# Optimization experiments

Measured on AMD Instinct MI355X. Metric: run time of the kernel, lower is better.

Reference implementation:

```python
import jax, jax.numpy as jnp
import numpy as np
from jax import lax

EPS = 1e-12
ALPHA = 20.0
TEMP = 10.0
TAU = 0.45
LAMBDA_N = 0.3
REP_W = 0.15
MOMENTUM = 0.9
N_SINK_ITER = 3


def _norm(x):
    # F.normalize(p=2, dim=1, eps=1e-12)
    return x / jnp.maximum(jnp.linalg.norm(x, axis=-1, keepdims=True), EPS)


def sinkhorn(sim, alpha=ALPHA, n_iterations=N_SINK_ITER):
    Q = jnp.exp(alpha * sim).T  # [K, B]
    K, B = Q.shape
    Q = Q / jnp.sum(Q)
    for _ in range(n_iterations):
        Q = Q / (jnp.sum(Q, axis=1, keepdims=True) * K)
        Q = Q / (jnp.sum(Q, axis=0, keepdims=True) * B)
    return (Q * B).T  # [B, K]


def update_negative_centers(n_feats, positive_center, negative_centers):
    # all under no_grad in the original
    nf = _norm(n_feats)
    pos = _norm(positive_center)
    sim_to_pos = (nf @ pos.T)[:, 0]                       # [Nn]
    keep = sim_to_pos < 0.7
    negc = _norm(negative_centers)
    sim = nf @ negc.T                                     # [Nn, K]
    assign = jnp.argmax(sim, axis=1)
    K = negative_centers.shape[0]
    onehot = jax.nn.one_hot(assign, K, dtype=n_feats.dtype) * keep[:, None].astype(n_feats.dtype)
    counts = jnp.sum(onehot, axis=0)                      # [K]
    sums = onehot.T @ n_feats                             # [K, D] masked per-cluster sums of raw feats
    means = sums / jnp.maximum(counts[:, None], 1.0)
    new_center = _norm(means)
    lerped = negative_centers + (new_center - negative_centers) * (1.0 - MOMENTUM)
    lerped = lerped / jnp.maximum(jnp.linalg.norm(lerped, axis=1, keepdims=True), EPS)
    # update only clusters with >=3 assigned kept features (skips everything if keep.sum()==0)
    return jnp.where((counts >= 3.0)[:, None], lerped, negative_centers)


def setup_inputs() -> dict:
    key = jax.random.key(0)
    ks = jax.random.split(key, 6)
    dim, n_proxies, n_centers = 512, 1024, 4
    return {
        'p_feats': jax.random.normal(ks[0], (16384, dim), jnp.float32),
        'u_feats': jax.random.normal(ks[1], (65536, dim), jnp.float32),
        'n_feats': jax.random.normal(ks[2], (32768, dim), jnp.float32),
        'positive_center': _norm(jax.random.normal(ks[3], (1, dim), jnp.float32)),
        'proxy_u': jax.random.normal(ks[4], (n_proxies, dim), jnp.float32),
        'negative_centers': _norm(jax.random.normal(ks[5], (n_centers, dim), jnp.float32)),
    }


def reference(p_feats, u_feats, n_feats, positive_center, proxy_u, negative_centers):
    pos = lax.stop_gradient(positive_center)   # requires_grad=False param
    negc0 = lax.stop_gradient(negative_centers)  # buffer

    # l_loss: mean(1 - cos(pos, p_feats))
    dist = _norm(pos) @ _norm(p_feats).T       # [1, Np]
    l_loss = jnp.mean(1.0 - dist)

    # EMA update of negative centers (no_grad)
    negc = lax.stop_gradient(update_negative_centers(lax.stop_gradient(n_feats), pos, negc0))

    # n branch: self-distillation on negative centers
    sim_n = _norm(n_feats) @ _norm(negc).T     # [Nn, K]
    target_n = jax.nn.softmax(sim_n, axis=1)
    loss_n = -jnp.mean(jnp.sum(target_n * jax.nn.log_softmax(sim_n, axis=1), axis=1))

    # pseudo-label branch on u_feats vs negative centers (sinkhorn targets, detached)
    sim_u_neg = _norm(u_feats) @ _norm(negc).T  # [Nu, K]
    soft_assign = sinkhorn(lax.stop_gradient(sim_u_neg))
    loss_pseudo = -jnp.mean(jnp.sum(soft_assign * jax.nn.log_softmax(sim_u_neg, axis=1), axis=1))

    n_loss = (loss_n + loss_pseudo) / 2.0

    # u branch vs learnable proxies
    u_similarity = _norm(u_feats) @ _norm(proxy_u).T  # [Nu, P]
    u_target = sinkhorn(lax.stop_gradient(u_similarity))
    u_loss = -jnp.mean(jnp.sum(u_target * jax.nn.log_softmax(u_similarity * TEMP, axis=1), axis=1))

    # repulsion
    sim_np = (_norm(negc) @ _norm(pos).T)[:, 0]       # [K]
    rep_np = -jnp.mean(jnp.log(jnp.clip(1.0 - sim_np, 1e-6, None)))
    nc = _norm(negc)
    sim_nn = nc @ nc.T                                 # [K, K]
    K = negc.shape[0]
    offdiag = ~jnp.eye(K, dtype=bool)
    logs = jnp.where(offdiag, jnp.log(jnp.clip(1.0 - sim_nn, 1e-6, None)), 0.0)
    rep_nn = -jnp.sum(logs) / (K * K - K)
    repulsion_loss = rep_np + 0.1 * rep_nn

    cls_loss = TAU * l_loss + LAMBDA_N * n_loss + (0.55 - TAU) * u_loss + REP_W * repulsion_loss
    return cls_loss, l_loss, u_loss, n_loss, repulsion_loss
```

## Files before the change

### kernel.cpp

```cpp
#include <hip/hip_runtime.h>
#include <hip/hip_bf16.h>

typedef __attribute__((ext_vector_type(8))) short short8;
typedef __attribute__((ext_vector_type(8))) unsigned short ushort8;
typedef __attribute__((ext_vector_type(4))) float f32x4;

#define EPSN 1e-12f
#define GN 1024
#define GK 512

__device__ __forceinline__ float bf2f(unsigned short h) {
  union { unsigned int u; float f; } c; c.u = ((unsigned int)h) << 16; return c.f;
}
__device__ __forceinline__ unsigned short f2bf(float f) {
  union { float f; unsigned int u; } c; c.f = f;
  unsigned int u = c.u;
  return (unsigned short)((u + 0x7fffu + ((u >> 16) & 1u)) >> 16);
}
__device__ __forceinline__ float wredsum(float v) {
  v += __shfl_xor(v, 32); v += __shfl_xor(v, 16); v += __shfl_xor(v, 8);
  v += __shfl_xor(v, 4);  v += __shfl_xor(v, 2);  v += __shfl_xor(v, 1);
  return v;
}

#define GLL(g, l) __builtin_amdgcn_global_load_lds( \
    (const __attribute__((address_space(1))) unsigned int*)(g), \
    (__attribute__((address_space(3))) unsigned int*)(l), 16, 0, 0)

__global__ void k_prep(const float* __restrict__ pc, const float* __restrict__ nc,
                       float* __restrict__ pos_hat, float* __restrict__ negc0_hat) {
  int tid = threadIdx.x, lane = tid & 63, w = tid >> 6;
  const float* src = (w == 0) ? pc : (nc + (w - 1) * 512);
  float* dst = (w == 0) ? pos_hat : (negc0_hat + (w - 1) * 512);
  float4 a = *(const float4*)(src + lane * 8);
  float4 b = *(const float4*)(src + lane * 8 + 4);
  float x[8] = {a.x,a.y,a.z,a.w,b.x,b.y,b.z,b.w};
  float ss = 0.f;
  #pragma unroll
  for (int j = 0; j < 8; j++) ss += x[j]*x[j];
  ss = wredsum(ss);
  float inv = 1.f / fmaxf(sqrtf(ss), EPSN);
  #pragma unroll
  for (int j = 0; j < 8; j++) dst[lane*8+j] = x[j]*inv;
}

__global__ __launch_bounds__(256) void k_redcol(const float* __restrict__ P, float* __restrict__ R,
                                                int nrows, int ncols) {
  __shared__ float lred[64];
  int tid = threadIdx.x, lane = tid & 63, w = tid >> 6;
  int colg = blockIdx.x * 16;
  int ci = tid & 15;
  int r0 = tid >> 4;
  float s = 0.f;
  for (int r = r0; r < nrows; r += 16)
    s += P[(size_t)r * ncols + colg + ci];
  s += __shfl_xor(s, 16); s += __shfl_xor(s, 32);
  if (lane < 16) lred[w * 16 + lane] = s;
  __syncthreads();
  if (tid < 16) R[colg + tid] = lred[tid] + lred[16 + tid] + lred[32 + tid] + lred[48 + tid];
}

__global__ __launch_bounds__(256) void k_rownormP(const float* __restrict__ X,
                                                  unsigned short* __restrict__ Y,
                                                  float* __restrict__ invn, int rows) {
  int lane = threadIdx.x & 63;
  int w0 = blockIdx.x * 4 + (threadIdx.x >> 6);
  int nw = gridDim.x * 4;
  for (int row = w0; row < rows; row += nw) {
    const float* src = X + (size_t)row * 512 + lane * 8;
    float4 a = *(const float4*)src;
    float4 b = *(const float4*)(src + 4);
    float x[8] = {a.x,a.y,a.z,a.w,b.x,b.y,b.z,b.w};
    float ss = 0.f;
    #pragma unroll
    for (int j = 0; j < 8; j++) ss += x[j]*x[j];
    ss = wredsum(ss);
    float inv = 1.f / fmaxf(sqrtf(ss), EPSN);
    if (lane == 0) invn[row] = inv;
    ushort8 o;
    #pragma unroll
    for (int j = 0; j < 8; j++) o[j] = f2bf(x[j]);
    *(ushort8*)(Y + (size_t)row * 512 + lane * 8) = o;
  }
}

__global__ __launch_bounds__(256) void k_ploss(const float* __restrict__ PF, const float* __restrict__ ph_g,
                                               float* __restrict__ PlossP) {
  __shared__ float lred[4];
  int tid = threadIdx.x, lane = tid & 63, w = tid >> 6;
  float ph[8];
  #pragma unroll
  for (int j = 0; j < 8; j++) ph[j] = ph_g[lane*8+j];
  float lsum = 0.f;
  int row0 = blockIdx.x * 32;
  for (int rr = w; rr < 32; rr += 4) {
    int row = row0 + rr;
    const float* src = PF + (size_t)row * 512 + lane * 8;
    float4 a = *(const float4*)src;
    float4 b = *(const float4*)(src + 4);
    float x[8] = {a.x,a.y,a.z,a.w,b.x,b.y,b.z,b.w};
    float ss = 0.f, dp = 0.f;
    #pragma unroll
    for (int j = 0; j < 8; j++) { ss += x[j]*x[j]; dp += x[j]*ph[j]; }
    ss = wredsum(ss); dp = wredsum(dp);
    if (lane == 0) lsum += dp / fmaxf(sqrtf(ss), EPSN);
  }
  if (lane == 0) lred[w] = lsum;
  __syncthreads();
  if (tid == 0) PlossP[blockIdx.x] = lred[0]+lred[1]+lred[2]+lred[3];
}

__global__ __launch_bounds__(256) void k_nstats(const float* __restrict__ NF, const float* __restrict__ ph_g,
                                                const float* __restrict__ nch0, float* __restrict__ inv_n,
                                                float* __restrict__ CntP, float* __restrict__ SumP) {
  __shared__ float fl[8192];
  __shared__ float cb[16];
  int tid = threadIdx.x, lane = tid & 63, w = tid >> 6;
  float ph[8], nh[4][8];
  #pragma unroll
  for (int j = 0; j < 8; j++) ph[j] = ph_g[lane*8+j];
  #pragma unroll
  for (int c = 0; c < 4; c++)
    #pragma unroll
    for (int j = 0; j < 8; j++) nh[c][j] = nch0[c*512 + lane*8 + j];
  float acc[4][8];
  float cnt[4] = {0.f,0.f,0.f,0.f};
  #pragma unroll
  for (int c = 0; c < 4; c++)
    #pragma unroll
    for (int j = 0; j < 8; j++) acc[c][j] = 0.f;
  int row0 = blockIdx.x * 64;
  for (int rr = w; rr < 64; rr += 4) {
    int row = row0 + rr;
    const float* src = NF + (size_t)row * 512 + lane * 8;
    float4 a = *(const float4*)src;
    float4 b = *(const float4*)(src + 4);
    float x[8] = {a.x,a.y,a.z,a.w,b.x,b.y,b.z,b.w};
    float ss = 0.f, dp = 0.f, dn[4] = {0.f,0.f,0.f,0.f};
    #pragma unroll
    for (int j = 0; j < 8; j++) {
      ss += x[j]*x[j]; dp += x[j]*ph[j];
      #pragma unroll
      for (int c = 0; c < 4; c++) dn[c] += x[j]*nh[c][j];
    }
    ss = wredsum(ss); dp = wredsum(dp);
    #pragma unroll
    for (int c = 0; c < 4; c++) dn[c] = wredsum(dn[c]);
    float inv = 1.f / fmaxf(sqrtf(ss), EPSN);
    if (lane == 0) inv_n[row] = inv;
    float sp = dp * inv;
    float s0 = dn[0]*inv, s1 = dn[1]*inv, s2 = dn[2]*inv, s3 = dn[3]*inv;
    int am = 0; float best = s0;
    if (s1 > best) { best = s1; am = 1; }
    if (s2 > best) { best = s2; am = 2; }
    if (s3 > best) { best = s3; am = 3; }
    float kf = (sp < 0.7f) ? 1.f : 0.f;
    #pragma unroll
    for (int c = 0; c < 4; c++) {
      float m = (am == c) ? kf : 0.f;
      #pragma unroll
      for (int j = 0; j < 8; j++) acc[c][j] += m * x[j];
      if (lane == 0) cnt[c] += m;
    }
  }
  #pragma unroll
  for (int c = 0; c < 4; c++)
    #pragma unroll
    for (int j = 0; j < 8; j++) fl[w*2048 + c*512 + lane*8 + j] = acc[c][j];
  if (lane == 0) {
    #pragma unroll
    for (int c = 0; c < 4; c++) cb[w*4+c] = cnt[c];
  }
  __syncthreads();
  for (int q = tid; q < 2048; q += 256)
    SumP[(size_t)blockIdx.x * 2048 + q] = fl[q] + fl[2048+q] + fl[4096+q] + fl[6144+q];
  if (tid < 4) CntP[blockIdx.x * 4 + tid] = cb[tid] + cb[4+tid] + cb[8+tid] + cb[12+tid];
}

__global__ void k_center(const float* __restrict__ CntP, const float* __restrict__ sums,
                         const float* __restrict__ negc_raw, const float* __restrict__ pos_hat,
                         float* __restrict__ negc_hat, float* __restrict__ scal) {
  __shared__ float hbuf[2048];
  __shared__ float spn[4];
  __shared__ float snn[16];
  int tid = threadIdx.x, lane = tid & 63, c = tid >> 6;
  float cs = 0.f;
  for (int r = lane; r < 512; r += 64) cs += CntP[r*4 + c];
  float cnt = wredsum(cs);
  float x[8], raw[8], ph[8];
  #pragma unroll
  for (int j = 0; j < 8; j++) {
    x[j] = sums[c*512 + lane*8 + j] / fmaxf(cnt, 1.f);
    raw[j] = negc_raw[c*512 + lane*8 + j];
    ph[j] = pos_hat[lane*8 + j];
  }
  float ss = 0.f;
  #pragma unroll
  for (int j = 0; j < 8; j++) ss += x[j]*x[j];
  ss = wredsum(ss);
  float n1 = fmaxf(sqrtf(ss), EPSN);
  #pragma unroll
  for (int j = 0; j < 8; j++) x[j] = raw[j] + (x[j]/n1 - raw[j]) * 0.1f;
  ss = 0.f;
  #pragma unroll
  for (int j = 0; j < 8; j++) ss += x[j]*x[j];
  ss = wredsum(ss);
  float n2 = fmaxf(sqrtf(ss), EPSN);
  bool upd = (cnt >= 3.0f);
  #pragma unroll
  for (int j = 0; j < 8; j++) x[j] = upd ? (x[j]/n2) : raw[j];
  ss = 0.f;
  #pragma unroll
  for (int j = 0; j < 8; j++) ss += x[j]*x[j];
  ss = wredsum(ss);
  float n3 = fmaxf(sqrtf(ss), EPSN);
  float dp = 0.f;
  #pragma unroll
  for (int j = 0; j < 8; j++) {
    x[j] = x[j] / n3;
    negc_hat[c*512 + lane*8 + j] = x[j];
    hbuf[c*512 + lane*8 + j] = x[j];
    dp += x[j] * ph[j];
  }
  dp = wredsum(dp);
  if (lane == 0) spn[c] = dp;
  __syncthreads();
  float d4[4] = {0.f,0.f,0.f,0.f};
  #pragma unroll
  for (int c2 = 0; c2 < 4; c2++) {
    float d = 0.f;
    #pragma unroll
    for (int j = 0; j < 8; j++) d += x[j] * hbuf[c2*512 + lane*8 + j];
    d4[c2] = wredsum(d);
  }
  if (lane == 0) {
    #pragma unroll
    for (int c2 = 0; c2 < 4; c2++) snn[c*4 + c2] = d4[c2];
  }
  __syncthreads();
  if (tid == 0) {
    float rep_np = 0.f;
    for (int i = 0; i < 4; i++) rep_np += logf(fmaxf(1.f - spn[i], 1e-6f));
    rep_np = -rep_np * 0.25f;
    float rep_nn = 0.f;
    for (int i = 0; i < 4; i++)
      for (int j2 = 0; j2 < 4; j2++)
        if (i != j2) rep_nn += logf(fmaxf(1.f - snn[i*4+j2], 1e-6f));
    rep_nn = -rep_nn / 12.f;
    scal[4] = rep_np + 0.1f * rep_nn;
  }
}

__global__ __launch_bounds__(256) void k_nloss(const float* __restrict__ NF, const float* __restrict__ inv_n,
                                               const float* __restrict__ nch, float* __restrict__ NlossP) {
  __shared__ float lred[4];
  int tid = threadIdx.x, lane = tid & 63, w = tid >> 6;
  float nh[4][8];
  #pragma unroll
  for (int c = 0; c < 4; c++)
    #pragma unroll
    for (int j = 0; j < 8; j++) nh[c][j] = nch[c*512 + lane*8 + j];
  float lsum = 0.f;
  int row0 = blockIdx.x * 32;
  for (int rr = w; rr < 32; rr += 4) {
    int row = row0 + rr;
    const float* src = NF + (size_t)row * 512 + lane * 8;
    float4 a = *(const float4*)src;
    float4 b = *(const float4*)(src + 4);
    float x[8] = {a.x,a.y,a.z,a.w,b.x,b.y,b.z,b.w};
    float dn[4] = {0.f,0.f,0.f,0.f};
    #pragma unroll
    for (int j = 0; j < 8; j++)
      #pragma unroll
      for (int c = 0; c < 4; c++) dn[c] += x[j]*nh[c][j];
    #pragma unroll
    for (int c = 0; c < 4; c++) dn[c] = wredsum(dn[c]);
    if (lane == 0) {
      float inv = inv_n[row];
      float s0 = dn[0]*inv, s1 = dn[1]*inv, s2 = dn[2]*inv, s3 = dn[3]*inv;
      float mx = fmaxf(fmaxf(s0,s1), fmaxf(s2,s3));
      float e0 = __expf(s0-mx), e1 = __expf(s1-mx), e2 = __expf(s2-mx), e3 = __expf(s3-mx);
      float Z = e0+e1+e2+e3;
      lsum += (mx + logf(Z)) - (e0*s0+e1*s1+e2*s2+e3*s3)/Z;
    }
  }
  if (lane == 0) lred[w] = lsum;
  __syncthreads();
  if (tid == 0) NlossP[blockIdx.x] = lred[0]+lred[1]+lred[2]+lred[3];
}

__global__ __launch_bounds__(256) void k_upass(const float* __restrict__ U, const float* __restrict__ nch,
                                               float* __restrict__ SU, float* __restrict__ UPp,
                                               unsigned short* __restrict__ Uh, float* __restrict__ invU) {
  __shared__ float ub[16];
  int tid = threadIdx.x, lane = tid & 63, w = tid >> 6;
  float nh[4][8];
  #pragma unroll
  for (int c = 0; c < 4; c++)
    #pragma unroll
    for (int j = 0; j < 8; j++) nh[c][j] = nch[c*512 + lane*8 + j];
  float eacc[4] = {0.f,0.f,0.f,0.f};
  int row0 = blockIdx.x * 32;
  for (int rr = w; rr < 32; rr += 4) {
    int row = row0 + rr;
    const float* src = U + (size_t)row * 512 + lane * 8;
    float4 a = *(const float4*)src;
    float4 b = *(const float4*)(src + 4);
    float x[8] = {a.x,a.y,a.z,a.w,b.x,b.y,b.z,b.w};
    float ss = 0.f, dn[4] = {0.f,0.f,0.f,0.f};
    #pragma unroll
    for (int j = 0; j < 8; j++) {
      ss += x[j]*x[j];
      #pragma unroll
      for (int c = 0; c < 4; c++) dn[c] += x[j]*nh[c][j];
    }
    ss = wredsum(ss);
    #pragma unroll
    for (int c = 0; c < 4; c++) dn[c] = wredsum(dn[c]);
    float inv = 1.f / fmaxf(sqrtf(ss), EPSN);
    ushort8 o;
    #pragma unroll
    for (int j = 0; j < 8; j++) o[j] = f2bf(x[j]);
    *(ushort8*)(Uh + (size_t)row * 512 + lane * 8) = o;
    if (lane == 0) {
      invU[row] = inv;
      float4 sv; sv.x = dn[0]*inv; sv.y = dn[1]*inv; sv.z = dn[2]*inv; sv.w = dn[3]*inv;
      *(float4*)(SU + (size_t)row * 4) = sv;
      eacc[0] += __expf(20.f*sv.x); eacc[1] += __expf(20.f*sv.y);
      eacc[2] += __expf(20.f*sv.z); eacc[3] += __expf(20.f*sv.w);
    }
  }
  if (lane == 0) {
    #pragma unroll
    for (int c = 0; c < 4; c++) ub[w*4+c] = eacc[c];
  }
  __syncthreads();
  if (tid < 4) UPp[blockIdx.x * 4 + tid] = ub[tid] + ub[4+tid] + ub[8+tid] + ub[12+tid];
}

__global__ __launch_bounds__(256) void k_psink(const float* __restrict__ SU, const float* __restrict__ Pin,
                                               int n_in, float* __restrict__ Pout,
                                               float* __restrict__ PLout, int mode) {
  __shared__ float lr[16];
  int tid = threadIdx.x, lane = tid & 63, w = tid >> 6;
  float i0 = 0.f, i1 = 0.f, i2 = 0.f, i3 = 0.f;
  for (int r = tid; r < n_in; r += 256) {
    float4 v = *(const float4*)(Pin + (size_t)r * 4);
    i0 += v.x; i1 += v.y; i2 += v.z; i3 += v.w;
  }
  i0 = wredsum(i0); i1 = wredsum(i1); i2 = wredsum(i2); i3 = wredsum(i3);
  if (lane == 0) { lr[w*4+0] = i0; lr[w*4+1] = i1; lr[w*4+2] = i2; lr[w*4+3] = i3; }
  __syncthreads();
  float R0 = lr[0]+lr[4]+lr[8]+lr[12];
  float R1_ = lr[1]+lr[5]+lr[9]+lr[13];
  float R2_ = lr[2]+lr[6]+lr[10]+lr[14];
  float R3_ = lr[3]+lr[7]+lr[11]+lr[15];
  float r0 = 1.f/(4.f*R0), r1 = 1.f/(4.f*R1_), r2 = 1.f/(4.f*R2_), r3 = 1.f/(4.f*R3_);
  float a0 = 0.f, a1 = 0.f, a2 = 0.f, a3 = 0.f, lsum = 0.f;
  int row = blockIdx.x * blockDim.x + threadIdx.x;
  {
    float4 s = *(const float4*)(SU + (size_t)row * 4);
    float x0 = __expf(20.f*s.x), x1 = __expf(20.f*s.y);
    float x2 = __expf(20.f*s.z), x3 = __expf(20.f*s.w);
    float E0 = x0*r0, E1 = x1*r1, E2 = x2*r2, E3 = x3*r3;
    float cf = 1.f / ((E0+E1+E2+E3) * 65536.f);
    if (mode == 1) { a0 = x0*cf; a1 = x1*cf; a2 = x2*cf; a3 = x3*cf; }
    else {
      float term = (E0*s.x + E1*s.y + E2*s.z + E3*s.w) * 65536.f * cf;
      float mx = fmaxf(fmaxf(s.x,s.y), fmaxf(s.z,s.w));
      float z = __expf(s.x-mx)+__expf(s.y-mx)+__expf(s.z-mx)+__expf(s.w-mx);
      lsum = (mx + logf(z)) - term;
    }
  }
  __syncthreads();
  if (mode == 1) {
    a0 = wredsum(a0); a1 = wredsum(a1); a2 = wredsum(a2); a3 = wredsum(a3);
    if (lane == 0) { lr[w*4+0] = a0; lr[w*4+1] = a1; lr[w*4+2] = a2; lr[w*4+3] = a3; }
    __syncthreads();
    if (tid < 4) Pout[blockIdx.x * 4 + tid] = lr[tid] + lr[4+tid] + lr[8+tid] + lr[12+tid];
  } else {
    lsum = wredsum(lsum);
    if (lane == 0) lr[w] = lsum;
    __syncthreads();
    if (tid == 0) PLout[blockIdx.x] = lr[0]+lr[1]+lr[2]+lr[3];
  }
}

__global__ __launch_bounds__(256) void k_gemm(const unsigned short* __restrict__ A,
                                              const unsigned short* __restrict__ B,
                                              const float* __restrict__ invU,
                                              const float* __restrict__ invP,
                                              unsigned short* __restrict__ S,
                                              float* __restrict__ R1) {
  __shared__ unsigned short lAB[17408];
  __shared__ float red[512];
  unsigned short* lA = lAB;
  unsigned short* lB = lAB + 8192;
  const int swz = (blockIdx.x & 7) * 512 + (blockIdx.x >> 3);
  const int rowblk = swz >> 3, colblk = swz & 7;
  const int tid = threadIdx.x, lane = tid & 63;
  const int wid = tid >> 6, wm = wid >> 1, wn = wid & 1;
  f32x4 acc[4][4];
  #pragma unroll
  for (int m = 0; m < 4; m++)
    #pragma unroll
    for (int n = 0; n < 4; n++) acc[m][n] = (f32x4){0.f,0.f,0.f,0.f};
  const unsigned short* Ag = A + (size_t)rowblk * 128 * GK;
  const unsigned short* Bg = B + (size_t)colblk * 128 * GK;
  const int r0 = tid >> 3;
  const int c0 = ((tid & 7) ^ (r0 & 7)) * 8;
  for (int kt = 0; kt < GK; kt += 64) {
    #pragma unroll
    for (int i = 0; i < 4; i++)
      GLL(Ag + (size_t)(r0 + i*32) * GK + kt + c0, lA + (i*256 + tid) * 8);
    #pragma unroll
    for (int i = 0; i < 4; i++)
      GLL(Bg + (size_t)(r0 + i*32) * GK + kt + c0, lB + (i*256 + tid) * 8);
    __syncthreads();
    #pragma unroll
    for (int kk = 0; kk < 2; kk++) {
      short8 af[4], bf[4];
      #pragma unroll
      for (int m = 0; m < 4; m++) {
        int rowA = wm*64 + m*16 + (lane & 15);
        int ch = ((kk*4 + (lane >> 4)) ^ (rowA & 7)) * 8;
        af[m] = *(const short8*)(lA + rowA * 64 + ch);
      }
      #pragma unroll
      for (int n = 0; n < 4; n++) {
        int rowB = wn*64 + n*16 + (lane & 15);
        int ch = ((kk*4 + (lane >> 4)) ^ (rowB & 7)) * 8;
        bf[n] = *(const short8*)(lB + rowB * 64 + ch);
      }
      #pragma unroll
      for (int m = 0; m < 4; m++)
        #pragma unroll
        for (int n = 0; n < 4; n++)
          acc[m][n] = __builtin_amdgcn_mfma_f32_16x16x32_bf16(af[m], bf[n], acc[m][n], 0, 0, 0);
    }
    __syncthreads();
  }
  unsigned short* lC = lAB;
  #pragma unroll
  for (int m = 0; m < 4; m++)
    #pragma unroll
    for (int n = 0; n < 4; n++) {
      int col = wn*64 + n*16 + (lane & 15);
      float ip = invP[colblk * 128 + col];
      #pragma unroll
      for (int r = 0; r < 4; r++) {
        int row = wm*64 + m*16 + ((lane >> 4) << 2) + r;
        float iu = invU[rowblk * 128 + row];
        lC[row * 136 + col] = f2bf(acc[m][n][r] * iu * ip);
      }
    }
  __syncthreads();
  float racc[16];
  #pragma unroll
  for (int j = 0; j < 16; j++) racc[j] = 0.f;
  const size_t outbase = (size_t)rowblk * 128 * GN + (size_t)colblk * 128;
  const int ch8 = lane & 7;
  const int rsub = lane >> 3;
  #pragma unroll
  for (int it = 0; it < 4; it++) {
    int row = it * 32 + wid * 8 + rsub;
    ushort8 v0 = *(const ushort8*)(lC + row * 136 + ch8 * 8);
    ushort8 v1 = *(const ushort8*)(lC + row * 136 + 64 + ch8 * 8);
    *(short8*)(S + outbase + (size_t)row * GN + ch8 * 8) = (short8)v0;
    *(short8*)(S + outbase + (size_t)row * GN + 64 + ch8 * 8) = (short8)v1;
    #pragma unroll
    for (int j = 0; j < 8; j++) {
      racc[j]     += __expf(20.f * bf2f(v0[j]));
      racc[8 + j] += __expf(20.f * bf2f(v1[j]));
    }
  }
  #pragma unroll
  for (int j = 0; j < 16; j++) {
    racc[j] += __shfl_xor(racc[j], 8);
    racc[j] += __shfl_xor(racc[j], 16);
    racc[j] += __shfl_xor(racc[j], 32);
  }
  if (lane < 8) {
    #pragma unroll
    for (int j = 0; j < 8; j++) {
      red[wid * 128 + lane * 8 + j]      = racc[j];
      red[wid * 128 + 64 + lane * 8 + j] = racc[8 + j];
    }
  }
  __syncthreads();
  if (tid < 128) {
    float s4 = red[tid] + red[128 + tid] + red[256 + tid] + red[384 + tid];
    int gcol = colblk * 128 + tid;
    int q = (gcol & 15) * 64 + (gcol >> 4);
    atomicAdd(&R1[q], s4);
  }
}

__global__ __launch_bounds__(256) void k_sink(const unsigned short* __restrict__ S,
                                              const float* __restrict__ Rin,
                                              float* __restrict__ Pout, float* __restrict__ LPout, int mode) {
  __shared__ float lds[4096];
  int tid = threadIdx.x, lane = tid & 63, w = tid >> 6;
  float rj[16];
  #pragma unroll
  for (int j = 0; j < 16; j++) rj[j] = 1.f / (1024.f * Rin[j*64 + lane]);
  float acc[16];
  #pragma unroll
  for (int j = 0; j < 16; j++) acc[j] = 0.f;
  float lsum = 0.f;
  int row0 = blockIdx.x * 32;
  for (int rr = w; rr < 32; rr += 4) {
    int row = row0 + rr;
    const unsigned short* Sr = S + (size_t)row * 1024 + lane * 16;
    ushort8 v0 = *(const ushort8*)Sr;
    ushort8 v1 = *(const ushort8*)(Sr + 8);
    float s[16], X[16], E[16];
    #pragma unroll
    for (int j = 0; j < 8; j++) { s[j] = bf2f(v0[j]); s[8+j] = bf2f(v1[j]); }
    float cs = 0.f;
    #pragma unroll
    for (int j = 0; j < 16; j++) { X[j] = __expf(20.f*s[j]); E[j] = X[j] * rj[j]; cs += E[j]; }
    cs = wredsum(cs);
    float cf = 1.f / (cs * 65536.f);
    if (mode == 1) {
      #pragma unroll
      for (int j = 0; j < 16; j++) acc[j] += X[j] * cf;
    } else {
      float term = 0.f, mx = -1e30f;
      #pragma unroll
      for (int j = 0; j < 16; j++) { term += E[j]*s[j]; mx = fmaxf(mx, s[j]); }
      term = wredsum(term);
      mx = fmaxf(mx, __shfl_xor(mx, 32)); mx = fmaxf(mx, __shfl_xor(mx, 16));
      mx = fmaxf(mx, __shfl_xor(mx, 8));  mx = fmaxf(mx, __shfl_xor(mx, 4));
      mx = fmaxf(mx, __shfl_xor(mx, 2));  mx = fmaxf(mx, __shfl_xor(mx, 1));
      float z = 0.f;
      #pragma unroll
      for (int j = 0; j < 16; j++) z += __expf(10.f*(s[j] - mx));
      z = wredsum(z);
      if (lane == 0) lsum += (10.f*mx + logf(z)) - term * (10.f * 65536.f * cf);
    }
  }
  if (mode == 1) {
    #pragma unroll
    for (int j = 0; j < 16; j++) lds[w*1024 + lane + 64*j] = acc[j];
    __syncthreads();
    for (int q = tid; q < 1024; q += 256)
      Pout[(size_t)blockIdx.x * 1024 + q] = lds[q] + lds[1024+q] + lds[2048+q] + lds[3072+q];
  } else {
    if (lane == 0) lds[w] = lsum;
    __syncthreads();
    if (tid == 0) LPout[blockIdx.x] = lds[0]+lds[1]+lds[2]+lds[3];
  }
}

__global__ __launch_bounds__(256) void k_final(const float* __restrict__ scal,
                                               const float* __restrict__ PlossP,
                                               const float* __restrict__ NlossP,
                                               const float* __restrict__ PLp,
                                               const float* __restrict__ SLp,
                                               float* __restrict__ out) {
  __shared__ float lr[4];
  int tid = threadIdx.x, lane = tid & 63, w = tid >> 6;
  float tots[4];
  const float* arrs[4] = {PlossP, NlossP, PLp, SLp};
  const int ns[4] = {512, 1024, 256, 2048};
  for (int k = 0; k < 4; k++) {
    float s = 0.f;
    for (int i = tid; i < ns[k]; i += 256) s += arrs[k][i];
    s = wredsum(s);
    __syncthreads();
    if (lane == 0) lr[w] = s;
    __syncthreads();
    tots[k] = lr[0]+lr[1]+lr[2]+lr[3];
  }
  if (tid == 0) {
    float l   = 1.f - tots[0] / 16384.f;
    float ln  = tots[1] / 32768.f;
    float lp  = tots[2] / 65536.f;
    float ul  = tots[3] / 65536.f;
    float rep = scal[4];
    float nl  = 0.5f * (ln + lp);
    float cls = 0.45f*l + 0.3f*nl + 0.1f*ul + 0.15f*rep;
    out[0] = cls;
    out[1] = l;
    out[2] = ul;
    out[3] = nl;
    out[4] = rep;
  }
}

extern "C" void kernel_launch(void* const* d_in, const int* in_sizes, int n_in,
                              void* d_out, int out_size, void* d_ws, size_t ws_size,
                              hipStream_t stream) {
  const float* PF = (const float*)d_in[0];
  const float* UF = (const float*)d_in[1];
  const float* NF = (const float*)d_in[2];
  const float* PC = (const float*)d_in[3];
  const float* PU = (const float*)d_in[4];
  const float* NC = (const float*)d_in[5];

  char* ws = (char*)d_ws;
  const size_t WS_REQUIRED = 202736768ULL;
  if (ws_size < WS_REQUIRED) return;

  float* R1     = (float*)(ws + 0);
  float* R2     = (float*)(ws + 4096);
  float* R3     = (float*)(ws + 8192);
  float* scal   = (float*)(ws + 12288);
  float* sums   = (float*)(ws + 12416);
  float* invP   = (float*)(ws + 20608);
  float* UPp    = (float*)(ws + 24704);
  float* PPpA   = (float*)(ws + 57472);
  float* PPpB   = (float*)(ws + 61568);
  float* PLp    = (float*)(ws + 65664);
  float* PlossP = (float*)(ws + 66688);
  float* NlossP = (float*)(ws + 68736);
  float* CntP   = (float*)(ws + 72832);
  float* pos_hat   = (float*)(ws + 81024);
  float* negc0_hat = (float*)(ws + 83072);
  float* negc_hat  = (float*)(ws + 91264);
  float* invU      = (float*)(ws + 99456);
  float* inv_n = (float*)(ws + 361600);
  float* SU    = (float*)(ws + 361600);
  unsigned short* Ph = (unsigned short*)(ws + 361600);
  float* SumP = (float*)(ws + 1410176);
  unsigned short* Uh = (unsigned short*)(ws + 1410176);
  float* SPp  = (float*)(ws + 1410176);
  float* SLp  = (float*)(ws + 9798784);
  unsigned short* S = (unsigned short*)(ws + 68519040);

  hipMemsetAsync(ws, 0, 4096, stream);

  k_prep<<<1, 320, 0, stream>>>(PC, NC, pos_hat, negc0_hat);
  k_ploss<<<512, 256, 0, stream>>>(PF, pos_hat, PlossP);
  k_nstats<<<512, 256, 0, stream>>>(NF, pos_hat, negc0_hat, inv_n, CntP, SumP);
  k_redcol<<<128, 256, 0, stream>>>(SumP, sums, 512, 2048);
  k_center<<<1, 256, 0, stream>>>(CntP, sums, NC, pos_hat, negc_hat, scal);
  k_nloss<<<1024, 256, 0, stream>>>(NF, inv_n, negc_hat, NlossP);
  k_upass<<<2048, 256, 0, stream>>>(UF, negc_hat, SU, UPp, Uh, invU);

  k_psink<<<256, 256, 0, stream>>>(SU, UPp, 2048, PPpA, nullptr, 1);
  k_psink<<<256, 256, 0, stream>>>(SU, PPpA, 256, PPpB, nullptr, 1);
  k_psink<<<256, 256, 0, stream>>>(SU, PPpB, 256, nullptr, PLp, 2);

  k_rownormP<<<4, 256, 0, stream>>>(PU, Ph, invP, 1024);

  k_gemm<<<4096, 256, 0, stream>>>(Uh, Ph, invU, invP, S, R1);
  k_sink<<<2048, 256, 0, stream>>>(S, R1, SPp, nullptr, 1);
  k_redcol<<<64, 256, 0, stream>>>(SPp, R2, 2048, 1024);
  k_sink<<<2048, 256, 0, stream>>>(S, R2, SPp, nullptr, 1);
  k_redcol<<<64, 256, 0, stream>>>(SPp, R3, 2048, 1024);
  k_sink<<<2048, 256, 0, stream>>>(S, R3, nullptr, SLp, 2);

  k_final<<<1, 256, 0, stream>>>(scal, PlossP, NlossP, PLp, SLp, (float*)d_out);
}
```

Measured before the change: 492.0 us.

## Enlarge GEMM tile to 256x128 and specialize sinkhorn kernels by mode

The similarity GEMM now uses 512-thread blocks computing 256x128 output tiles, so B tiles are reused across twice as many rows. The epilogue is staged in two halves through LDS. The sinkhorn kernel is split into a column-sum variant and a loss variant. Each processes two rows per iteration for more memory-level parallelism, and the loss variant computes exp(10s) once and squares it, dropping the max-subtraction in log-softmax. The extra rownorm blocks and the skipped max add occupancy and numerical-overflow risk in exchange for less redundant work.

```diff
diff --git a/kernel.cpp b/kernel.cpp
--- a/kernel.cpp
+++ b/kernel.cpp
@@ -386,17 +386,17 @@
   }
 }
 
-__global__ __launch_bounds__(256) void k_gemm(const unsigned short* __restrict__ A,
+__global__ __launch_bounds__(512) void k_gemm(const unsigned short* __restrict__ A,
                                               const unsigned short* __restrict__ B,
                                               const float* __restrict__ invU,
                                               const float* __restrict__ invP,
                                               unsigned short* __restrict__ S,
                                               float* __restrict__ R1) {
-  __shared__ unsigned short lAB[17408];
-  __shared__ float red[512];
+  __shared__ unsigned short lAB[24576];
+  __shared__ float red[1024];
   unsigned short* lA = lAB;
-  unsigned short* lB = lAB + 8192;
-  const int swz = (blockIdx.x & 7) * 512 + (blockIdx.x >> 3);
+  unsigned short* lB = lAB + 16384;
+  const int swz = (blockIdx.x & 7) * 256 + (blockIdx.x >> 3);
   const int rowblk = swz >> 3, colblk = swz & 7;
   const int tid = threadIdx.x, lane = tid & 63;
   const int wid = tid >> 6, wm = wid >> 1, wn = wid & 1;
@@ -405,17 +405,17 @@
   for (int m = 0; m < 4; m++)
     #pragma unroll
     for (int n = 0; n < 4; n++) acc[m][n] = (f32x4){0.f,0.f,0.f,0.f};
-  const unsigned short* Ag = A + (size_t)rowblk * 128 * GK;
+  const unsigned short* Ag = A + (size_t)rowblk * 256 * GK;
   const unsigned short* Bg = B + (size_t)colblk * 128 * GK;
   const int r0 = tid >> 3;
   const int c0 = ((tid & 7) ^ (r0 & 7)) * 8;
   for (int kt = 0; kt < GK; kt += 64) {
     #pragma unroll
     for (int i = 0; i < 4; i++)
-      GLL(Ag + (size_t)(r0 + i*32) * GK + kt + c0, lA + (i*256 + tid) * 8);
-    #pragma unroll
-    for (int i = 0; i < 4; i++)
-      GLL(Bg + (size_t)(r0 + i*32) * GK + kt + c0, lB + (i*256 + tid) * 8);
+      GLL(Ag + (size_t)(r0 + i*64) * GK + kt + c0, lA + (i*512 + tid) * 8);
+    #pragma unroll
+    for (int i = 0; i < 2; i++)
+      GLL(Bg + (size_t)(r0 + i*64) * GK + kt + c0, lB + (i*512 + tid) * 8);
     __syncthreads();
     #pragma unroll
     for (int kk = 0; kk < 2; kk++) {
@@ -441,38 +441,44 @@
     __syncthreads();
   }
   unsigned short* lC = lAB;
-  #pragma unroll
-  for (int m = 0; m < 4; m++)
-    #pragma unroll
-    for (int n = 0; n < 4; n++) {
-      int col = wn*64 + n*16 + (lane & 15);
-      float ip = invP[colblk * 128 + col];
-      #pragma unroll
-      for (int r = 0; r < 4; r++) {
-        int row = wm*64 + m*16 + ((lane >> 4) << 2) + r;
-        float iu = invU[rowblk * 128 + row];
-        lC[row * 136 + col] = f2bf(acc[m][n][r] * iu * ip);
+  float racc[16];
+  #pragma unroll
+  for (int j = 0; j < 16; j++) racc[j] = 0.f;
+  const size_t outbase = (size_t)rowblk * 256 * GN + (size_t)colblk * 128;
+  const int ch8 = lane & 7, rsub = lane >> 3;
+  #pragma unroll
+  for (int h = 0; h < 2; h++) {
+    if ((wm >> 1) == h) {
+      #pragma unroll
+      for (int m = 0; m < 4; m++)
+        #pragma unroll
+        for (int n = 0; n < 4; n++) {
+          int col = wn*64 + n*16 + (lane & 15);
+          float ip = invP[colblk * 128 + col];
+          #pragma unroll
+          for (int r = 0; r < 4; r++) {
+            int lr2 = (wm & 1)*64 + m*16 + ((lane >> 4) << 2) + r;
+            float iu = invU[rowblk * 256 + h*128 + lr2];
+            lC[lr2 * 136 + col] = f2bf(acc[m][n][r] * iu * ip);
+          }
+        }
+    }
+    __syncthreads();
+    #pragma unroll
+    for (int it = 0; it < 2; it++) {
+      int lr2 = it*64 + wid*8 + rsub;
+      int grow = h*128 + lr2;
+      ushort8 v0 = *(const ushort8*)(lC + lr2 * 136 + ch8 * 8);
+      ushort8 v1 = *(const ushort8*)(lC + lr2 * 136 + 64 + ch8 * 8);
+      *(short8*)(S + outbase + (size_t)grow * GN + ch8 * 8) = (short8)v0;
+      *(short8*)(S + outbase + (size_t)grow * GN + 64 + ch8 * 8) = (short8)v1;
+      #pragma unroll
+      for (int j = 0; j < 8; j++) {
+        racc[j]     += __expf(20.f * bf2f(v0[j]));
+        racc[8 + j] += __expf(20.f * bf2f(v1[j]));
       }
     }
-  __syncthreads();
-  float racc[16];
-  #pragma unroll
-  for (int j = 0; j < 16; j++) racc[j] = 0.f;
-  const size_t outbase = (size_t)rowblk * 128 * GN + (size_t)colblk * 128;
-  const int ch8 = lane & 7;
-  const int rsub = lane >> 3;
-  #pragma unroll
-  for (int it = 0; it < 4; it++) {
-    int row = it * 32 + wid * 8 + rsub;
-    ushort8 v0 = *(const ushort8*)(lC + row * 136 + ch8 * 8);
-    ushort8 v1 = *(const ushort8*)(lC + row * 136 + 64 + ch8 * 8);
-    *(short8*)(S + outbase + (size_t)row * GN + ch8 * 8) = (short8)v0;
-    *(short8*)(S + outbase + (size_t)row * GN + 64 + ch8 * 8) = (short8)v1;
-    #pragma unroll
-    for (int j = 0; j < 8; j++) {
-      racc[j]     += __expf(20.f * bf2f(v0[j]));
-      racc[8 + j] += __expf(20.f * bf2f(v1[j]));
-    }
+    __syncthreads();
   }
   #pragma unroll
   for (int j = 0; j < 16; j++) {
@@ -489,16 +495,18 @@
   }
   __syncthreads();
   if (tid < 128) {
-    float s4 = red[tid] + red[128 + tid] + red[256 + tid] + red[384 + tid];
+    float s8 = 0.f;
+    #pragma unroll
+    for (int i = 0; i < 8; i++) s8 += red[i * 128 + tid];
     int gcol = colblk * 128 + tid;
     int q = (gcol & 15) * 64 + (gcol >> 4);
-    atomicAdd(&R1[q], s4);
-  }
-}
-
-__global__ __launch_bounds__(256) void k_sink(const unsigned short* __restrict__ S,
-                                              const float* __restrict__ Rin,
-                                              float* __restrict__ Pout, float* __restrict__ LPout, int mode) {
+    atomicAdd(&R1[q], s8);
+  }
+}
+
+__global__ __launch_bounds__(256) void k_sink1(const unsigned short* __restrict__ S,
+                                               const float* __restrict__ Rin,
+                                               float* __restrict__ Pout) {
   __shared__ float lds[4096];
   int tid = threadIdx.x, lane = tid & 63, w = tid >> 6;
   float rj[16];
@@ -507,50 +515,82 @@
   float acc[16];
   #pragma unroll
   for (int j = 0; j < 16; j++) acc[j] = 0.f;
+  int row0 = blockIdx.x * 32;
+  for (int rr = w; rr < 16; rr += 4) {
+    const unsigned short* SrA = S + (size_t)(row0 + rr) * 1024 + lane * 16;
+    const unsigned short* SrB = S + (size_t)(row0 + rr + 16) * 1024 + lane * 16;
+    ushort8 a0 = *(const ushort8*)SrA, a1 = *(const ushort8*)(SrA + 8);
+    ushort8 b0 = *(const ushort8*)SrB, b1 = *(const ushort8*)(SrB + 8);
+    float XA[16], XB[16];
+    float csA = 0.f, csB = 0.f;
+    #pragma unroll
+    for (int j = 0; j < 8; j++) {
+      XA[j]   = __expf(20.f * bf2f(a0[j]));
+      XA[8+j] = __expf(20.f * bf2f(a1[j]));
+      XB[j]   = __expf(20.f * bf2f(b0[j]));
+      XB[8+j] = __expf(20.f * bf2f(b1[j]));
+    }
+    #pragma unroll
+    for (int j = 0; j < 16; j++) { csA += XA[j]*rj[j]; csB += XB[j]*rj[j]; }
+    #pragma unroll
+    for (int d = 32; d >= 1; d >>= 1) {
+      csA += __shfl_xor(csA, d);
+      csB += __shfl_xor(csB, d);
+    }
+    float cfA = 1.f / (csA * 65536.f), cfB = 1.f / (csB * 65536.f);
+    #pragma unroll
+    for (int j = 0; j < 16; j++) acc[j] += XA[j]*cfA + XB[j]*cfB;
+  }
+  #pragma unroll
+  for (int j = 0; j < 16; j++) lds[w*1024 + lane + 64*j] = acc[j];
+  __syncthreads();
+  for (int q = tid; q < 1024; q += 256)
+    Pout[(size_t)blockIdx.x * 1024 + q] = lds[q] + lds[1024+q] + lds[2048+q] + lds[3072+q];
+}
+
+__global__ __launch_bounds__(256) void k_sinkL(const unsigned short* __restrict__ S,
+                                               const float* __restrict__ Rin,
+                                               float* __restrict__ LPout) {
+  __shared__ float lr[4];
+  int tid = threadIdx.x, lane = tid & 63, w = tid >> 6;
+  float rj[16];
+  #pragma unroll
+  for (int j = 0; j < 16; j++) rj[j] = 1.f / (1024.f * Rin[j*64 + lane]);
   float lsum = 0.f;
   int row0 = blockIdx.x * 32;
-  for (int rr = w; rr < 32; rr += 4) {
-    int row = row0 + rr;
-    const unsigned short* Sr = S + (size_t)row * 1024 + lane * 16;
-    ushort8 v0 = *(const ushort8*)Sr;
-    ushort8 v1 = *(const ushort8*)(Sr + 8);
-    float s[16], X[16], E[16];
-    #pragma unroll
-    for (int j = 0; j < 8; j++) { s[j] = bf2f(v0[j]); s[8+j] = bf2f(v1[j]); }
-    float cs = 0.f;
-    #pragma unroll
-    for (int j = 0; j < 16; j++) { X[j] = __expf(20.f*s[j]); E[j] = X[j] * rj[j]; cs += E[j]; }
-    cs = wredsum(cs);
-    float cf = 1.f / (cs * 65536.f);
-    if (mode == 1) {
-      #pragma unroll
-      for (int j = 0; j < 16; j++) acc[j] += X[j] * cf;
-    } else {
-      float term = 0.f, mx = -1e30f;
-      #pragma unroll
-      for (int j = 0; j < 16; j++) { term += E[j]*s[j]; mx = fmaxf(mx, s[j]); }
-      term = wredsum(term);
-      mx = fmaxf(mx, __shfl_xor(mx, 32)); mx = fmaxf(mx, __shfl_xor(mx, 16));
-      mx = fmaxf(mx, __shfl_xor(mx, 8));  mx = fmaxf(mx, __shfl_xor(mx, 4));
-      mx = fmaxf(mx, __shfl_xor(mx, 2));  mx = fmaxf(mx, __shfl_xor(mx, 1));
-      float z = 0.f;
-      #pragma unroll
-      for (int j = 0; j < 16; j++) z += __expf(10.f*(s[j] - mx));
-      z = wredsum(z);
-      if (lane == 0) lsum += (10.f*mx + logf(z)) - term * (10.f * 65536.f * cf);
-    }
-  }
-  if (mode == 1) {
-    #pragma unroll
-    for (int j = 0; j < 16; j++) lds[w*1024 + lane + 64*j] = acc[j];
-    __syncthreads();
-    for (int q = tid; q < 1024; q += 256)
-      Pout[(size_t)blockIdx.x * 1024 + q] = lds[q] + lds[1024+q] + lds[2048+q] + lds[3072+q];
-  } else {
-    if (lane == 0) lds[w] = lsum;
-    __syncthreads();
-    if (tid == 0) LPout[blockIdx.x] = lds[0]+lds[1]+lds[2]+lds[3];
-  }
+  for (int rr = w; rr < 16; rr += 4) {
+    const unsigned short* SrA = S + (size_t)(row0 + rr) * 1024 + lane * 16;
+    const unsigned short* SrB = S + (size_t)(row0 + rr + 16) * 1024 + lane * 16;
+    ushort8 a0 = *(const ushort8*)SrA, a1 = *(const ushort8*)(SrA + 8);
+    ushort8 b0 = *(const ushort8*)SrB, b1 = *(const ushort8*)(SrB + 8);
+    float sA[16], sB[16], yA[16], yB[16];
+    #pragma unroll
+    for (int j = 0; j < 8; j++) {
+      sA[j] = bf2f(a0[j]); sA[8+j] = bf2f(a1[j]);
+      sB[j] = bf2f(b0[j]); sB[8+j] = bf2f(b1[j]);
+    }
+    #pragma unroll
+    for (int j = 0; j < 16; j++) { yA[j] = __expf(10.f*sA[j]); yB[j] = __expf(10.f*sB[j]); }
+    float csA = 0.f, csB = 0.f, tA = 0.f, tB = 0.f, YA = 0.f, YB = 0.f;
+    #pragma unroll
+    for (int j = 0; j < 16; j++) {
+      float xa = yA[j]*yA[j]*rj[j];
+      float xb = yB[j]*yB[j]*rj[j];
+      csA += xa; tA += xa*sA[j]; YA += yA[j];
+      csB += xb; tB += xb*sB[j]; YB += yB[j];
+    }
+    #pragma unroll
+    for (int d = 32; d >= 1; d >>= 1) {
+      csA += __shfl_xor(csA, d); csB += __shfl_xor(csB, d);
+      tA  += __shfl_xor(tA, d);  tB  += __shfl_xor(tB, d);
+      YA  += __shfl_xor(YA, d);  YB  += __shfl_xor(YB, d);
+    }
+    if (lane == 0)
+      lsum += (logf(YA) - 10.f*tA/csA) + (logf(YB) - 10.f*tB/csB);
+  }
+  if (lane == 0) lr[w] = lsum;
+  __syncthreads();
+  if (tid == 0) LPout[blockIdx.x] = lr[0]+lr[1]+lr[2]+lr[3];
 }
 
 __global__ __launch_bounds__(256) void k_final(const float* __restrict__ scal,
@@ -643,14 +683,14 @@
   k_psink<<<256, 256, 0, stream>>>(SU, PPpA, 256, PPpB, nullptr, 1);
   k_psink<<<256, 256, 0, stream>>>(SU, PPpB, 256, nullptr, PLp, 2);
 
-  k_rownormP<<<4, 256, 0, stream>>>(PU, Ph, invP, 1024);
-
-  k_gemm<<<4096, 256, 0, stream>>>(Uh, Ph, invU, invP, S, R1);
-  k_sink<<<2048, 256, 0, stream>>>(S, R1, SPp, nullptr, 1);
+  k_rownormP<<<32, 256, 0, stream>>>(PU, Ph, invP, 1024);
+
+  k_gemm<<<2048, 512, 0, stream>>>(Uh, Ph, invU, invP, S, R1);
+  k_sink1<<<2048, 256, 0, stream>>>(S, R1, SPp);
   k_redcol<<<64, 256, 0, stream>>>(SPp, R2, 2048, 1024);
-  k_sink<<<2048, 256, 0, stream>>>(S, R2, SPp, nullptr, 1);
+  k_sink1<<<2048, 256, 0, stream>>>(S, R2, SPp);
   k_redcol<<<64, 256, 0, stream>>>(SPp, R3, 2048, 1024);
-  k_sink<<<2048, 256, 0, stream>>>(S, R3, nullptr, SLp, 2);
+  k_sinkL<<<2048, 256, 0, stream>>>(S, R3, SLp);
 
   k_final<<<1, 256, 0, stream>>>(scal, PlossP, NlossP, PLp, SLp, (float*)d_out);
 }
```

New measurement: 419.0 us. -14.8%, faster.
